# Kernel optimization log

Hardware: AMD Instinct MI355X
Metric: run time of the kernel (lower is better)

Reference implementation:

```python
import jax, jax.numpy as jnp
import numpy as np

B, H, D = 32, 64, 128          # batch (decode), indexer heads, head dim
PAGE, PAGES = 64, 128          # cache page size, pages per sequence
S = PAGE * PAGES               # max kv len = 8192
NUM_PAGES = B * PAGES          # 4096 pages total
TOPK = 2048
SCALE = float(D) ** -0.5
FILL = -1


def setup_inputs() -> dict:
    key = jax.random.key(0)
    ks = jax.random.split(key, 6)
    q = jax.random.normal(ks[0], (B, H, D), dtype=jnp.float32)
    k = jax.random.normal(ks[1], (B, D), dtype=jnp.float32)          # current-step key
    weights = jax.random.uniform(ks[2], (B, H), dtype=jnp.float32)   # per-head gates
    # fp8 cache emulated as quantized values (k_cache) x per-token scales (k_s_cache)
    k_cache = jax.random.normal(ks[3], (NUM_PAGES, PAGE, D), dtype=jnp.float32)
    k_s_cache = jax.random.uniform(ks[4], (NUM_PAGES, PAGE), minval=0.5, maxval=1.5, dtype=jnp.float32)
    kv_seqlens = jax.random.randint(ks[5], (B,), S // 2, S + 1, dtype=jnp.int32)
    block_offsets = jnp.arange(NUM_PAGES, dtype=jnp.int32).reshape(B, PAGES)
    return dict(q=q, k=k, weights=weights, k_cache=k_cache, k_s_cache=k_s_cache,
                kv_seqlens=kv_seqlens, block_offsets=block_offsets)


def reference(q, k, weights, k_cache, k_s_cache, kv_seqlens, block_offsets):
    # Gather paged cache per sequence and dequantize: [B, S, D]
    kv = k_cache[block_offsets].reshape(B, S, D) * k_s_cache[block_offsets].reshape(B, S, 1)
    pos = jnp.arange(S, dtype=jnp.int32)
    # Current step's key lives at position kv_len - 1
    cur = pos[None, :] == (kv_seqlens[:, None] - 1)
    kv = jnp.where(cur[..., None], k[:, None, :], kv)
    # Indexer score: sum_h w[b,h] * relu(q[b,h] . k[b,s]) * scale
    logits = jnp.einsum('bhd,bsd->bhs', q, kv) * SCALE
    scores = jnp.einsum('bh,bhs->bs', weights, jax.nn.relu(logits))  # [B, S]
    valid = pos[None, :] < kv_seqlens[:, None]
    scores = jnp.where(valid, scores, -jnp.inf)
    vals, idx = jax.lax.top_k(scores, TOPK)
    idx = jnp.where(jnp.isfinite(vals), idx, FILL).astype(jnp.int32)
    return idx, scores
```

## Files before the change

### kernel.cpp

```cpp
#include <hip/hip_runtime.h>
#include <hip/hip_bf16.h>
#include <math.h>

#define NB 32
#define NH 64
#define ND 128
#define PAGE_SZ 64
#define NPAGES 128
#define NS 8192
#define NTOPK 2048
#define QSCALE 0.08838834764831845f
#define NEG_SENTINEL -3.0e38f

typedef __attribute__((ext_vector_type(8))) short short8;
typedef __attribute__((ext_vector_type(4))) float f32x4;

static __device__ __forceinline__ unsigned pack2(float x, float y) {
    union { __hip_bfloat162 h; unsigned u; } c;
    c.h = __float22bfloat162_rn(make_float2(x, y));
    return c.u;
}

static __device__ __forceinline__ short8 pack8(const float4 &a, const float4 &b) {
    union { unsigned u[4]; short8 s; } c;
    c.u[0] = pack2(a.x, a.y);
    c.u[1] = pack2(a.z, a.w);
    c.u[2] = pack2(b.x, b.y);
    c.u[3] = pack2(b.z, b.w);
    return c.s;
}

__global__ __launch_bounds__(256, 4) void score_kernel(
    const float* __restrict__ q,
    const float* __restrict__ kcur,
    const float* __restrict__ w,
    const float* __restrict__ kc,
    const float* __restrict__ ksc,
    const int*   __restrict__ kvlen,
    const int*   __restrict__ bo,
    float* __restrict__ scores_out)
{
    __shared__ __align__(16) unsigned short q_lds[64 * 128];
    __shared__ float w_lds[NH];

    const int b    = blockIdx.y;
    const int sb   = blockIdx.x;
    const int t    = threadIdx.x;
    const int wv   = t >> 6;
    const int lane = t & 63;
    const int len  = kvlen[b];
    const int cur  = len - 1;
    const int s_base = sb * 128;

    if (s_base >= len) {
        if (t < 128)
            scores_out[(size_t)b * NS + s_base + t] = NEG_SENTINEL;
        return;
    }

    const int tok = wv * 16 + (lane & 15);
    const int l4  = lane >> 4;

    float4 gA[8];
    float  scA;

#define LOADP(P)                                                              \
    {                                                                         \
        int pg = bo[b * NPAGES + sb * 2 + (P)];                               \
        int tg = s_base + (P) * 64 + tok;                                     \
        bool iscur = (tg == cur);                                             \
        const float* kb = iscur ? (kcur + (size_t)b * ND)                     \
                                : (kc + (size_t)pg * (PAGE_SZ * ND) +         \
                                   (size_t)tok * ND);                         \
        scA = iscur ? 1.0f : ksc[pg * PAGE_SZ + tok];                         \
        _Pragma("unroll")                                                     \
        for (int ki = 0; ki < 4; ++ki) {                                      \
            gA[2 * ki]     = *(const float4*)(kb + ki * 32 + l4 * 8);         \
            gA[2 * ki + 1] = *(const float4*)(kb + ki * 32 + l4 * 8 + 4);     \
        }                                                                     \
    }

    LOADP(0)

    const float* qb = q + (size_t)b * NH * ND;
#pragma unroll
    for (int i = 0; i < 8; ++i) {
        int f = t + 256 * i;
        int row = f >> 5, d4 = f & 31;
        float4 v = *(const float4*)(qb + row * ND + d4 * 4);
        unsigned lo = pack2(v.x, v.y);
        unsigned hi = pack2(v.z, v.w);
        int ck = (d4 >> 1) ^ (row & 7);
        *(uint2*)(q_lds + row * 128 + (ck << 3) + (d4 & 1) * 4) = make_uint2(lo, hi);
    }
    if (t < NH) w_lds[t] = w[b * NH + t];
    __syncthreads();

    float wgt[4][4];
#pragma unroll
    for (int hb = 0; hb < 4; ++hb)
#pragma unroll
        for (int r = 0; r < 4; ++r)
            wgt[hb][r] = w_lds[hb * 16 + (lane >> 4) * 4 + r];

    const int arow = lane & 15;
    const int aswz = lane & 7;

#pragma unroll
    for (int p = 0; p < 2; ++p) {
        short8 bF[4];
#pragma unroll
        for (int ki = 0; ki < 4; ++ki) bF[ki] = pack8(gA[2 * ki], gA[2 * ki + 1]);
        const float scP = scA;

        if (p < 1) LOADP(p + 1)

        f32x4 acc[4];
#pragma unroll
        for (int hb = 0; hb < 4; ++hb) acc[hb] = (f32x4){0.f, 0.f, 0.f, 0.f};
#pragma unroll
        for (int ki = 0; ki < 4; ++ki) {
            const int ck = (ki * 4 + l4) ^ aswz;
#pragma unroll
            for (int hb = 0; hb < 4; ++hb) {
                short8 a = *(const short8*)(
                    q_lds + (hb * 16 + arow) * 128 + (ck << 3));
                acc[hb] = __builtin_amdgcn_mfma_f32_16x16x32_bf16(
                    a, bF[ki], acc[hb], 0, 0, 0);
            }
        }

        float part = 0.f;
#pragma unroll
        for (int hb = 0; hb < 4; ++hb)
#pragma unroll
            for (int r = 0; r < 4; ++r)
                part = fmaf(wgt[hb][r], fmaxf(acc[hb][r], 0.f), part);
        part += __shfl_xor(part, 16);
        part += __shfl_xor(part, 32);
        int sg = s_base + p * 64 + tok;
        if (l4 == 0) {
            float val = part * (scP * QSCALE);
            scores_out[(size_t)b * NS + sg] = (sg < len) ? val : NEG_SENTINEL;
        }
    }
#undef LOADP
}

static __device__ __forceinline__ void cex(unsigned &a, unsigned &b, bool desc) {
    unsigned lo = a < b ? a : b;
    unsigned hi = a < b ? b : a;
    a = desc ? hi : lo;
    b = desc ? lo : hi;
}

__global__ __launch_bounds__(256) void topk_sort(
    const float* __restrict__ scores,
    const int*   __restrict__ kvlen,
    unsigned* __restrict__ wsk)
{
    __shared__ unsigned keys[2048];
    const int b = blockIdx.y, c = blockIdx.x, t = threadIdx.x;
    unsigned* wrow = wsk + ((size_t)b * 4 + c) * 2048;

    if (c * 2048 >= kvlen[b]) {
#pragma unroll
        for (int r = 0; r < 8; ++r) wrow[t * 8 + r] = 0u;
        return;
    }

    const float* srow = scores + (size_t)b * NS + c * 2048;
    unsigned v[8];
    {
        float4 f0 = *(const float4*)(srow + t * 8);
        float4 f1 = *(const float4*)(srow + t * 8 + 4);
        float fv[8] = {f0.x, f0.y, f0.z, f0.w, f1.x, f1.y, f1.z, f1.w};
#pragma unroll
        for (int r = 0; r < 8; ++r) {
            int s = c * 2048 + t * 8 + r;
            float x = fv[r];
            v[r] = (x >= 0.f)
                 ? ((__float_as_uint(x) & 0xFFFFC000u) | (unsigned)(8192 - s))
                 : 0u;
        }
    }

    cex(v[0], v[1], true);  cex(v[2], v[3], false);
    cex(v[4], v[5], true);  cex(v[6], v[7], false);
    cex(v[0], v[2], true);  cex(v[1], v[3], true);
    cex(v[4], v[6], false); cex(v[5], v[7], false);
    cex(v[0], v[1], true);  cex(v[2], v[3], true);
    cex(v[4], v[5], false); cex(v[6], v[7], false);

    for (int k = 8; k <= 2048; k <<= 1) {
        const bool desc = (((unsigned)(t << 3)) & (unsigned)k) == 0u;
        for (int j = k >> 1; j >= 8; j >>= 1) {
            const int m = j >> 3;
            const bool keepHi = (((t & m) == 0) == desc);
            if (m < 64) {
#pragma unroll
                for (int r = 0; r < 8; ++r) {
                    unsigned o = __shfl_xor(v[r], m);
                    unsigned lo = v[r] < o ? v[r] : o;
                    unsigned hi = v[r] < o ? o : v[r];
                    v[r] = keepHi ? hi : lo;
                }
            } else {
                __syncthreads();
#pragma unroll
                for (int r = 0; r < 8; ++r) keys[t * 8 + r] = v[r];
                __syncthreads();
                const int pt = t ^ m;
#pragma unroll
                for (int r = 0; r < 8; ++r) {
                    unsigned o = keys[pt * 8 + r];
                    unsigned lo = v[r] < o ? v[r] : o;
                    unsigned hi = v[r] < o ? o : v[r];
                    v[r] = keepHi ? hi : lo;
                }
            }
        }
        cex(v[0], v[4], desc); cex(v[1], v[5], desc);
        cex(v[2], v[6], desc); cex(v[3], v[7], desc);
        cex(v[0], v[2], desc); cex(v[1], v[3], desc);
        cex(v[4], v[6], desc); cex(v[5], v[7], desc);
        cex(v[0], v[1], desc); cex(v[2], v[3], desc);
        cex(v[4], v[5], desc); cex(v[6], v[7], desc);
    }

#pragma unroll
    for (int r = 0; r < 8; ++r) wrow[t * 8 + r] = v[r];
}

__global__ __launch_bounds__(512) void topk_merge(
    const unsigned* __restrict__ wsk,
    int* __restrict__ idx_out)
{
    __shared__ unsigned keys[4096];
    const int b = blockIdx.x, t = threadIdx.x;
    const int g = t >> 8, tl = t & 255;
    const unsigned* base = wsk + (size_t)b * 4 * 2048;

    const unsigned* A = base + (2 * g) * 2048;
    const unsigned* B = base + (2 * g + 1) * 2048;
    unsigned v[8];
#pragma unroll
    for (int r = 0; r < 8; ++r) {
        int i = tl * 8 + r;
        unsigned a = A[i], bb = B[2047 - i];
        v[r] = a > bb ? a : bb;
    }
#pragma unroll
    for (int j = 1024; j >= 512; j >>= 1) {
        const int m = j >> 3;
        const bool keepHi = ((tl & m) == 0);
        __syncthreads();
#pragma unroll
        for (int r = 0; r < 8; ++r) keys[g * 2048 + tl * 8 + r] = v[r];
        __syncthreads();
        const int pt = tl ^ m;
#pragma unroll
        for (int r = 0; r < 8; ++r) {
            unsigned o = keys[g * 2048 + pt * 8 + r];
            unsigned lo = v[r] < o ? v[r] : o;
            unsigned hi = v[r] < o ? o : v[r];
            v[r] = keepHi ? hi : lo;
        }
    }
#pragma unroll
    for (int j = 256; j >= 8; j >>= 1) {
        const int m = j >> 3;
        const bool keepHi = ((tl & m) == 0);
#pragma unroll
        for (int r = 0; r < 8; ++r) {
            unsigned o = __shfl_xor(v[r], m);
            unsigned lo = v[r] < o ? v[r] : o;
            unsigned hi = v[r] < o ? o : v[r];
            v[r] = keepHi ? hi : lo;
        }
    }
    cex(v[0], v[4], true); cex(v[1], v[5], true);
    cex(v[2], v[6], true); cex(v[3], v[7], true);
    cex(v[0], v[2], true); cex(v[1], v[3], true);
    cex(v[4], v[6], true); cex(v[5], v[7], true);
    cex(v[0], v[1], true); cex(v[2], v[3], true);
    cex(v[4], v[5], true); cex(v[6], v[7], true);

    __syncthreads();
#pragma unroll
    for (int r = 0; r < 8; ++r) keys[g * 2048 + tl * 8 + r] = v[r];
    __syncthreads();

    unsigned u[4];
#pragma unroll
    for (int r = 0; r < 4; ++r) {
        int i = t * 4 + r;
        unsigned a = keys[i], bb = keys[2048 + 2047 - i];
        u[r] = a > bb ? a : bb;
    }
#pragma unroll
    for (int j = 1024; j >= 256; j >>= 1) {
        const int m = j >> 2;
        const bool keepHi = ((t & m) == 0);
        __syncthreads();
#pragma unroll
        for (int r = 0; r < 4; ++r) keys[t * 4 + r] = u[r];
        __syncthreads();
        const int pt = t ^ m;
#pragma unroll
        for (int r = 0; r < 4; ++r) {
            unsigned o = keys[pt * 4 + r];
            unsigned lo = u[r] < o ? u[r] : o;
            unsigned hi = u[r] < o ? o : u[r];
            u[r] = keepHi ? hi : lo;
        }
    }
#pragma unroll
    for (int j = 128; j >= 4; j >>= 1) {
        const int m = j >> 2;
        const bool keepHi = ((t & m) == 0);
#pragma unroll
        for (int r = 0; r < 4; ++r) {
            unsigned o = __shfl_xor(u[r], m);
            unsigned lo = u[r] < o ? u[r] : o;
            unsigned hi = u[r] < o ? o : u[r];
            u[r] = keepHi ? hi : lo;
        }
    }
    cex(u[0], u[2], true); cex(u[1], u[3], true);
    cex(u[0], u[1], true); cex(u[2], u[3], true);

#pragma unroll
    for (int r = 0; r < 4; ++r) {
        unsigned key = u[r];
        idx_out[b * NTOPK + t * 4 + r] =
            key ? (int)(8192u - (key & 0x3FFFu)) : -1;
    }
}

extern "C" void kernel_launch(void* const* d_in, const int* in_sizes, int n_in,
                              void* d_out, int out_size, void* d_ws, size_t ws_size,
                              hipStream_t stream)
{
    const float* q     = (const float*)d_in[0];
    const float* kcur  = (const float*)d_in[1];
    const float* w     = (const float*)d_in[2];
    const float* kc    = (const float*)d_in[3];
    const float* ksc   = (const float*)d_in[4];
    const int*   kvlen = (const int*)d_in[5];
    const int*   bo    = (const int*)d_in[6];

    int*      idx_out    = (int*)d_out;
    float*    scores_out = (float*)d_out + (size_t)NB * NTOPK;
    unsigned* wsk        = (unsigned*)d_ws;

    score_kernel<<<dim3(64, NB), 256, 0, stream>>>(q, kcur, w, kc, ksc, kvlen,
                                                   bo, scores_out);
    topk_sort<<<dim3(4, NB), 256, 0, stream>>>(scores_out, kvlen, wsk);
    topk_merge<<<NB, 512, 0, stream>>>(wsk, idx_out);
}
```

Measured before the change: 43.37 us.

## Coalesce KV page loads and stage bf16 tiles through LDS

After: 44.60 us. 1.03x slower.

```diff
diff --git a/kernel.cpp b/kernel.cpp
--- a/kernel.cpp
+++ b/kernel.cpp
@@ -19,15 +19,6 @@
     union { __hip_bfloat162 h; unsigned u; } c;
     c.h = __float22bfloat162_rn(make_float2(x, y));
     return c.u;
-}
-
-static __device__ __forceinline__ short8 pack8(const float4 &a, const float4 &b) {
-    union { unsigned u[4]; short8 s; } c;
-    c.u[0] = pack2(a.x, a.y);
-    c.u[1] = pack2(a.z, a.w);
-    c.u[2] = pack2(b.x, b.y);
-    c.u[3] = pack2(b.z, b.w);
-    return c.s;
 }
 
 __global__ __launch_bounds__(256, 4) void score_kernel(
@@ -41,6 +32,7 @@
     float* __restrict__ scores_out)
 {
     __shared__ __align__(16) unsigned short q_lds[64 * 128];
+    __shared__ __align__(16) unsigned short kv_lds[2 * 64 * 128];
     __shared__ float w_lds[NH];
 
     const int b    = blockIdx.y;
@@ -58,29 +50,35 @@
         return;
     }
 
-    const int tok = wv * 16 + (lane & 15);
-    const int l4  = lane >> 4;
-
-    float4 gA[8];
-    float  scA;
-
-#define LOADP(P)                                                              \
+    const int l5 = lane & 31;
+
+    float4 gA[8], gB[8];
+#define LOADPG(P, G)                                                          \
     {                                                                         \
         int pg = bo[b * NPAGES + sb * 2 + (P)];                               \
-        int tg = s_base + (P) * 64 + tok;                                     \
-        bool iscur = (tg == cur);                                             \
-        const float* kb = iscur ? (kcur + (size_t)b * ND)                     \
-                                : (kc + (size_t)pg * (PAGE_SZ * ND) +         \
-                                   (size_t)tok * ND);                         \
-        scA = iscur ? 1.0f : ksc[pg * PAGE_SZ + tok];                         \
+        const float* kb = kc + (size_t)pg * (PAGE_SZ * ND);                   \
         _Pragma("unroll")                                                     \
-        for (int ki = 0; ki < 4; ++ki) {                                      \
-            gA[2 * ki]     = *(const float4*)(kb + ki * 32 + l4 * 8);         \
-            gA[2 * ki + 1] = *(const float4*)(kb + ki * 32 + l4 * 8 + 4);     \
+        for (int i = 0; i < 8; ++i) {                                         \
+            int tokL = wv * 16 + i * 2 + (lane >> 5);                         \
+            bool iscur = (s_base + (P) * 64 + tokL) == cur;                   \
+            const float* src = iscur                                          \
+                ? (kcur + (size_t)b * ND + l5 * 4)                            \
+                : (kb + wv * 2048 + i * 256 + lane * 4);                      \
+            G[i] = *(const float4*)src;                                       \
         }                                                                     \
     }
-
-    LOADP(0)
+    LOADPG(0, gA)
+    LOADPG(1, gB)
+
+    const int tokP = wv * 16 + (lane & 15);
+    const int l4   = lane >> 4;
+    float scP[2];
+#pragma unroll
+    for (int p = 0; p < 2; ++p) {
+        int pg = bo[b * NPAGES + sb * 2 + p];
+        bool iscur = (s_base + p * 64 + tokP) == cur;
+        scP[p] = iscur ? 1.0f : ksc[pg * PAGE_SZ + tokP];
+    }
 
     const float* qb = q + (size_t)b * NH * ND;
 #pragma unroll
@@ -94,6 +92,24 @@
         *(uint2*)(q_lds + row * 128 + (ck << 3) + (d4 & 1) * 4) = make_uint2(lo, hi);
     }
     if (t < NH) w_lds[t] = w[b * NH + t];
+
+#define STAGE(G, P)                                                           \
+    {                                                                         \
+        _Pragma("unroll")                                                     \
+        for (int i = 0; i < 8; ++i) {                                         \
+            int tokL = wv * 16 + i * 2 + (lane >> 5);                         \
+            unsigned lo = pack2(G[i].x, G[i].y);                              \
+            unsigned hi = pack2(G[i].z, G[i].w);                              \
+            int ch = (l5 >> 1) ^ (tokL & 7);                                  \
+            *(uint2*)(kv_lds + (P) * 8192 + tokL * 128 + ch * 8 +             \
+                      (lane & 1) * 4) = make_uint2(lo, hi);                   \
+        }                                                                     \
+    }
+    STAGE(gA, 0)
+    STAGE(gB, 1)
+#undef LOADPG
+#undef STAGE
+
     __syncthreads();
 
     float wgt[4][4];
@@ -101,7 +117,7 @@
     for (int hb = 0; hb < 4; ++hb)
 #pragma unroll
         for (int r = 0; r < 4; ++r)
-            wgt[hb][r] = w_lds[hb * 16 + (lane >> 4) * 4 + r];
+            wgt[hb][r] = w_lds[hb * 16 + l4 * 4 + r];
 
     const int arow = lane & 15;
     const int aswz = lane & 7;
@@ -110,10 +126,10 @@
     for (int p = 0; p < 2; ++p) {
         short8 bF[4];
 #pragma unroll
-        for (int ki = 0; ki < 4; ++ki) bF[ki] = pack8(gA[2 * ki], gA[2 * ki + 1]);
-        const float scP = scA;
-
-        if (p < 1) LOADP(p + 1)
+        for (int ki = 0; ki < 4; ++ki) {
+            int ch = (ki * 4 + l4) ^ (tokP & 7);
+            bF[ki] = *(const short8*)(kv_lds + p * 8192 + tokP * 128 + ch * 8);
+        }
 
         f32x4 acc[4];
 #pragma unroll
@@ -138,13 +154,12 @@
                 part = fmaf(wgt[hb][r], fmaxf(acc[hb][r], 0.f), part);
         part += __shfl_xor(part, 16);
         part += __shfl_xor(part, 32);
-        int sg = s_base + p * 64 + tok;
+        int sg = s_base + p * 64 + tokP;
         if (l4 == 0) {
-            float val = part * (scP * QSCALE);
+            float val = part * (scP[p] * QSCALE);
             scores_out[(size_t)b * NS + sg] = (sg < len) ? val : NEG_SENTINEL;
         }
     }
-#undef LOADP
 }
 
 static __device__ __forceinline__ void cex(unsigned &a, unsigned &b, bool desc) {
```
